# Optimization experiments

Hardware: AMD Instinct MI355X
Metric: run time of the kernel (lower is better)

Reference implementation:

```python
import jax, jax.numpy as jnp
import numpy as np

K = 1024      # num_embeddings
D = 256       # embedding_dim
BETA = 0.25


def setup_inputs() -> dict:
    key = jax.random.key(0)
    k1, k2 = jax.random.split(key)
    latents = jax.random.normal(k1, (32, D, 32, 32), dtype=jnp.float32)
    # nn.Embedding weight init: uniform(-1/K, 1/K)
    weight = jax.random.uniform(k2, (K, D), dtype=jnp.float32,
                                minval=-1.0 / K, maxval=1.0 / K)
    return {"latents": latents, "weight": weight}


def reference(latents, weight):
    # NCHW -> NHWC
    lat = jnp.transpose(latents, (0, 2, 3, 1))          # [B,H,W,D]
    lat_shape = lat.shape
    flat = lat.reshape(-1, D)                           # [N,D]

    dist = (jnp.sum(flat ** 2, axis=1, keepdims=True)
            - 2.0 * jnp.matmul(flat, weight.T)
            + jnp.sum(weight ** 2, axis=1))             # [N,K]

    min_ind = jnp.argmin(dist, axis=1)                  # [N]
    min_embed = jax.nn.one_hot(min_ind, K, dtype=flat.dtype)  # [N,K]

    # one-hot @ weight == direct gather
    z_q = jnp.take(weight, min_ind, axis=0).reshape(lat_shape)  # [B,H,W,D]

    sg = jax.lax.stop_gradient
    loss = (jnp.mean((sg(z_q) - lat) ** 2)
            + BETA * jnp.mean((z_q - sg(lat)) ** 2))

    # straight-through estimator
    z_q_st = lat + sg(z_q - lat)

    e_mean = jnp.mean(min_embed, axis=0)                # [K]
    perplexity = jnp.exp(-jnp.sum(e_mean * jnp.log(e_mean + 1e-10)))

    z_q_out = jnp.transpose(z_q_st, (0, 3, 1, 2))       # NHWC -> NCHW
    return (loss, z_q_out, perplexity, min_embed, min_ind[:, None])
```

## Files before the change

### kernel.cpp

```cpp
#include <hip/hip_runtime.h>

#define KN 1024
#define DD 256
#define NTOT 32768
#define HW 1024

#define OFF_LOSS 0
#define OFF_ZQ   1
#define OFF_PERP 8388609
#define OFF_EMB  8388610
#define OFF_IND  41943042

#define WS_WSUM2_OFF 4112
#define WS_WBH_OFF   8208
#define WS_WBL_OFF   (8208 + 524288)

#define XS_STRIDE 260
#define THR 3.0e-4f

typedef __bf16 bf16x8 __attribute__((ext_vector_type(8)));
typedef float  f32x4  __attribute__((ext_vector_type(4)));
typedef float  f32x2  __attribute__((ext_vector_type(2)));
typedef unsigned short ushort_t;

#define SM_XS    0
#define SM_XFH   33280
#define SM_XFL   49664
#define SM_WSC   66048
#define SM_PART  70144
#define SM_REDV  70144
#define SM_ROWM  71232
#define SM_CCNT  71360
#define SM_CLIST 71488
#define SM_FV    72512
#define SM_ASUM  73536
#define SM_BI    73664
#define SM_LRED  73792
#define SM_SIZE  73824

__device__ __forceinline__ unsigned short bf16_rne(float f) {
    unsigned u = __float_as_uint(f);
    return (unsigned short)((u + 0x7FFFu + ((u >> 16) & 1u)) >> 16);
}

__device__ __forceinline__ float exact_dist(const float* xs, const float* wsC,
                                            const float* asum,
                                            const float* __restrict__ w,
                                            int r, int k) {
    float a = 0.f;
    const float4* wr = (const float4*)(w + k * DD);
    const float4* xr = (const float4*)(xs + r * XS_STRIDE);
    #pragma unroll 4
    for (int q = 0; q < 64; ++q) {
        const float4 wv = wr[q];
        const float4 xv = xr[q];
        a = fmaf(xv.x, wv.x, a);
        a = fmaf(xv.y, wv.y, a);
        a = fmaf(xv.z, wv.z, a);
        a = fmaf(xv.w, wv.w, a);
    }
    return (asum[r] - 2.0f * a) + wsC[k];
}

__global__ __launch_bounds__(256) void vq_prep(const float* __restrict__ w,
                                               float* __restrict__ wsum2,
                                               ushort_t* __restrict__ wBh,
                                               ushort_t* __restrict__ wBl) {
    const int k = blockIdx.x;
    const int d = threadIdx.x;
    float v = w[k * DD + d];
    {
        const int c = k >> 4, s0 = d >> 5, g = (d >> 3) & 3, j = d & 7;
        const int lane = (k & 15) | (g << 4);
        const int idx = (((c * 8 + s0) * 64 + lane) << 3) + j;
        const unsigned short hh = bf16_rne(v);
        wBh[idx] = hh;
        wBl[idx] = bf16_rne(v - __uint_as_float((unsigned)hh << 16));
    }
    float s = v * v;
    #pragma unroll
    for (int off = 32; off; off >>= 1) s += __shfl_down(s, off, 64);
    __shared__ float wsum[4];
    const int wave = d >> 6, lane = d & 63;
    if (lane == 0) wsum[wave] = s;
    __syncthreads();
    if (d == 0) wsum2[k] = (wsum[0] + wsum[1]) + (wsum[2] + wsum[3]);
}

__global__ __launch_bounds__(512, 4) void vq_main(const float* __restrict__ lat,
                                                  const float* __restrict__ w,
                                                  const float* __restrict__ wsum2,
                                                  const ushort_t* __restrict__ wBh,
                                                  const ushort_t* __restrict__ wBl,
                                                  float* __restrict__ out,
                                                  unsigned* __restrict__ cnt,
                                                  double* __restrict__ lossSum) {
    extern __shared__ char smem[];
    float*    xs    = (float*)(smem + SM_XS);
    ushort_t* xfH   = (ushort_t*)(smem + SM_XFH);
    ushort_t* xfL   = (ushort_t*)(smem + SM_XFL);
    float*    wsC   = (float*)(smem + SM_WSC);
    float*    part  = (float*)(smem + SM_PART);
    float*    redv  = (float*)(smem + SM_REDV);
    float*    rowm  = (float*)(smem + SM_ROWM);
    unsigned* ccnt  = (unsigned*)(smem + SM_CCNT);
    int*      clist = (int*)(smem + SM_CLIST);
    float*    fv    = (float*)(smem + SM_FV);
    float*    asum  = (float*)(smem + SM_ASUM);
    int*      bi    = (int*)(smem + SM_BI);
    double*   lred  = (double*)(smem + SM_LRED);

    const int n0  = blockIdx.x * 32;
    const int b   = n0 >> 10;
    const int hw0 = n0 & 1023;
    const int tid = threadIdx.x;
    const int l   = tid & 63;
    const int wv  = tid >> 6;

    {
        const float* base = lat + (size_t)b * (DD * HW) + hw0;
        #pragma unroll
        for (int it = 0; it < 4; ++it) {
            const int u = it * 512 + tid;
            const int d = u >> 3, r4 = (u & 7) * 4;
            const f32x4 v = __builtin_nontemporal_load(
                reinterpret_cast<const f32x4*>(base + d * HW + r4));
            xs[(r4 + 0) * XS_STRIDE + d] = v.x;
            xs[(r4 + 1) * XS_STRIDE + d] = v.y;
            xs[(r4 + 2) * XS_STRIDE + d] = v.z;
            xs[(r4 + 3) * XS_STRIDE + d] = v.w;
        }
        wsC[tid] = wsum2[tid];
        wsC[tid + 512] = wsum2[tid + 512];
    }
    __syncthreads();

    #pragma unroll
    for (int h = 0; h < 2; ++h) {
        if (tid < 256) {
            const int r = tid & 15, seg = tid >> 4;
            float p = 0.f;
            #pragma unroll
            for (int i = 0; i < 16; ++i) {
                float x = xs[(h * 16 + r) * XS_STRIDE + seg * 16 + i];
                p += x * x;
            }
            part[seg * 17 + r] = p;
        }
        __syncthreads();
        if (tid < 16) {
            float a = 0.f;
            #pragma unroll
            for (int s = 0; s < 16; ++s) a += part[s * 17 + tid];
            asum[h * 16 + tid] = a;
        }
        __syncthreads();
    }

    #pragma unroll
    for (int i = 0; i < 2; ++i) {
        const int u  = tid + i * 512;
        const int rt = u >> 9, s0 = (u >> 6) & 7, ll = u & 63;
        const int row = rt * 16 + (ll & 15);
        const int d0  = s0 * 32 + (ll >> 4) * 8;
        const float4 x0 = *(const float4*)(xs + row * XS_STRIDE + d0);
        const float4 x1 = *(const float4*)(xs + row * XS_STRIDE + d0 + 4);
        float xv[8] = {x0.x, x0.y, x0.z, x0.w, x1.x, x1.y, x1.z, x1.w};
        unsigned hh[8], lo[8];
        #pragma unroll
        for (int j = 0; j < 8; ++j) {
            hh[j] = bf16_rne(xv[j]);
            lo[j] = bf16_rne(xv[j] - __uint_as_float(hh[j] << 16));
        }
        uint4 ph, pl;
        ph.x = hh[0] | (hh[1] << 16); ph.y = hh[2] | (hh[3] << 16);
        ph.z = hh[4] | (hh[5] << 16); ph.w = hh[6] | (hh[7] << 16);
        pl.x = lo[0] | (lo[1] << 16); pl.y = lo[2] | (lo[3] << 16);
        pl.z = lo[4] | (lo[5] << 16); pl.w = lo[6] | (lo[7] << 16);
        *(uint4*)(xfH + u * 8) = ph;
        *(uint4*)(xfL + u * 8) = pl;
    }
    __syncthreads();

    f32x4 acc[2][8];
    #pragma unroll
    for (int rt = 0; rt < 2; ++rt)
        #pragma unroll
        for (int c = 0; c < 8; ++c)
            acc[rt][c] = (f32x4){0.f, 0.f, 0.f, 0.f};

    {
        bf16x8 ah0, ah1, al0, al1;
        bf16x8 pbh0, pbl0, pbh1, pbl1;

        #define BOFF(s0_, c_) (((size_t)(((wv * 8 + (c_)) * 8 + (s0_)) * 64 + l)) * 8)
        pbh0 = *(const bf16x8*)(wBh + BOFF(0, 0));
        pbl0 = *(const bf16x8*)(wBl + BOFF(0, 0));
        pbh1 = *(const bf16x8*)(wBh + BOFF(0, 1));
        pbl1 = *(const bf16x8*)(wBl + BOFF(0, 1));

        #pragma unroll
        for (int it = 0; it < 64; ++it) {
            const int s0 = it >> 3, c = it & 7;
            if (c == 0) {
                ah0 = *(const bf16x8*)(xfH + ((0 * 8 + s0) * 64 + l) * 8);
                ah1 = *(const bf16x8*)(xfH + ((1 * 8 + s0) * 64 + l) * 8);
                al0 = *(const bf16x8*)(xfL + ((0 * 8 + s0) * 64 + l) * 8);
                al1 = *(const bf16x8*)(xfL + ((1 * 8 + s0) * 64 + l) * 8);
            }
            bf16x8 bh, bl;
            if ((it & 1) == 0) { bh = pbh0; bl = pbl0; } else { bh = pbh1; bl = pbl1; }
            if (it + 2 < 64) {
                const int nit = it + 2, ns = nit >> 3, nc = nit & 7;
                if ((it & 1) == 0) {
                    pbh0 = *(const bf16x8*)(wBh + BOFF(ns, nc));
                    pbl0 = *(const bf16x8*)(wBl + BOFF(ns, nc));
                } else {
                    pbh1 = *(const bf16x8*)(wBh + BOFF(ns, nc));
                    pbl1 = *(const bf16x8*)(wBl + BOFF(ns, nc));
                }
            }
            acc[0][c] = __builtin_amdgcn_mfma_f32_16x16x32_bf16(ah0, bh, acc[0][c], 0, 0, 0);
            acc[1][c] = __builtin_amdgcn_mfma_f32_16x16x32_bf16(ah1, bh, acc[1][c], 0, 0, 0);
            acc[0][c] = __builtin_amdgcn_mfma_f32_16x16x32_bf16(ah0, bl, acc[0][c], 0, 0, 0);
            acc[1][c] = __builtin_amdgcn_mfma_f32_16x16x32_bf16(ah1, bl, acc[1][c], 0, 0, 0);
            acc[0][c] = __builtin_amdgcn_mfma_f32_16x16x32_bf16(al0, bh, acc[0][c], 0, 0, 0);
            acc[1][c] = __builtin_amdgcn_mfma_f32_16x16x32_bf16(al1, bh, acc[1][c], 0, 0, 0);
        }
        #undef BOFF
    }

    float rmv[2][4];
    #pragma unroll
    for (int rt = 0; rt < 2; ++rt)
        #pragma unroll
        for (int q = 0; q < 4; ++q) rmv[rt][q] = 3.4e38f;
    #pragma unroll
    for (int c = 0; c < 8; ++c) {
        const float cv = wsC[(wv * 8 + c) * 16 + (l & 15)];
        #pragma unroll
        for (int rt = 0; rt < 2; ++rt) {
            #pragma unroll
            for (int q = 0; q < 4; ++q) {
                const float dv = fmaf(-2.0f, acc[rt][c][q], cv);
                acc[rt][c][q] = dv;
                rmv[rt][q] = fminf(rmv[rt][q], dv);
            }
        }
    }
    #pragma unroll
    for (int rt = 0; rt < 2; ++rt)
        #pragma unroll
        for (int q = 0; q < 4; ++q) {
            float m = rmv[rt][q];
            #pragma unroll
            for (int off = 1; off < 16; off <<= 1) m = fminf(m, __shfl_xor(m, off, 64));
            rmv[rt][q] = m;
        }
    if ((l & 15) == 0) {
        const int g = l >> 4;
        #pragma unroll
        for (int rt = 0; rt < 2; ++rt)
            #pragma unroll
            for (int q = 0; q < 4; ++q)
                redv[wv * 32 + rt * 16 + g * 4 + q] = rmv[rt][q];
    }
    __syncthreads();
    if (tid < 32) {
        float m = redv[tid];
        #pragma unroll
        for (int ww = 1; ww < 8; ++ww) m = fminf(m, redv[ww * 32 + tid]);
        rowm[tid] = m;
        ccnt[tid] = 0u;
    }
    __syncthreads();

    #pragma unroll
    for (int rt = 0; rt < 2; ++rt) {
        #pragma unroll
        for (int q = 0; q < 4; ++q) {
            const int row = rt * 16 + ((l >> 4) << 2) + q;
            const float lim = rowm[row] + THR;
            #pragma unroll
            for (int c = 0; c < 8; ++c) {
                if (acc[rt][c][q] <= lim) {
                    const unsigned pos = atomicAdd(&ccnt[row], 1u);
                    if (pos < 8) clist[row * 8 + pos] = (wv * 8 + c) * 16 + (l & 15);
                }
            }
        }
    }
    __syncthreads();

    if (tid < 256) {
        const int r = tid >> 3, ci = tid & 7;
        const unsigned cc = ccnt[r];
        if (cc >= 2u) {
            if (cc <= 8u) {
                if ((unsigned)ci < cc)
                    fv[r * 8 + ci] = exact_dist(xs, wsC, asum, w, r, clist[r * 8 + ci]);
            } else {
                float bvv = 3.4e38f; int bkk = ci * 128;
                for (int k = ci * 128; k < ci * 128 + 128; ++k) {
                    const float dvv = exact_dist(xs, wsC, asum, w, r, k);
                    if (dvv < bvv) { bvv = dvv; bkk = k; }
                }
                fv[r * 8 + ci] = bvv;
                clist[r * 8 + ci] = bkk;
            }
        }
    }
    __syncthreads();
    if (tid < 32) {
        const unsigned cc = ccnt[tid];
        int kk;
        if (cc == 1u) kk = clist[tid * 8];
        else {
            const unsigned ncand = (cc <= 8u) ? cc : 8u;
            float v = fv[tid * 8]; kk = clist[tid * 8];
            for (unsigned ci = 1; ci < ncand; ++ci) {
                const float ov = fv[tid * 8 + ci];
                const int   ok = clist[tid * 8 + ci];
                if (ov < v || (ov == v && ok < kk)) { v = ov; kk = ok; }
            }
        }
        bi[tid] = kk;
        __builtin_nontemporal_store((float)kk, &out[OFF_IND + n0 + tid]);
        atomicAdd(&cnt[kk], 1u);
    }
    __syncthreads();

    {
        float* zq_out = out + OFF_ZQ + (size_t)b * (DD * HW) + hw0;
        #pragma unroll
        for (int it = 0; it < 8; ++it) {
            const int u = it * 512 + tid;
            const int d = u >> 4, j2 = (u & 15) * 2;
            const float la0 = xs[(j2 + 0) * XS_STRIDE + d];
            const float la1 = xs[(j2 + 1) * XS_STRIDE + d];
            const float z0  = w[bi[j2 + 0] * DD + d];
            const float z1  = w[bi[j2 + 1] * DD + d];
            f32x2 v;
            v.x = la0 + (z0 - la0);
            v.y = la1 + (z1 - la1);
            __builtin_nontemporal_store(v, reinterpret_cast<f32x2*>(zq_out + d * HW + j2));
        }
    }

    {
        f32x2* emb2 = reinterpret_cast<f32x2*>(out + OFF_EMB) + (size_t)n0 * (KN / 2);
        #pragma unroll
        for (int it = 0; it < 32; ++it) {
            const int f = it * 512 + tid;
            const int r = f >> 9;
            const int kq = (f & 511) * 2;
            const int tt = bi[r];
            f32x2 v2;
            v2.x = (kq     == tt) ? 1.0f : 0.0f;
            v2.y = (kq + 1 == tt) ? 1.0f : 0.0f;
            __builtin_nontemporal_store(v2, &emb2[f]);
        }
    }

    #pragma unroll
    for (int h = 0; h < 2; ++h) {
        if (tid < 256) {
            const int jj = tid & 15, db = tid >> 4;
            const int krow = bi[h * 16 + jj];
            float lsum = 0.f;
            #pragma unroll
            for (int it = 0; it < 16; ++it) {
                const int d = it * 16 + db;
                const float latv = xs[(h * 16 + jj) * XS_STRIDE + d];
                const float zq   = w[krow * DD + d];
                const float dif  = zq - latv;
                lsum = fmaf(dif, dif, lsum);
            }
            float s2 = lsum;
            #pragma unroll
            for (int off = 32; off; off >>= 1) s2 += __shfl_down(s2, off, 64);
            if ((tid & 63) == 0) lred[wv] = (double)s2;
        }
        __syncthreads();
        if (tid == 0) {
            double t = (lred[0] + lred[1]) + (lred[2] + lred[3]);
            atomicAdd(lossSum, t);
        }
        __syncthreads();
    }
}

__global__ __launch_bounds__(1024) void vq_finalize(const unsigned* __restrict__ cnt,
                                                    const double* __restrict__ lossSum,
                                                    float* __restrict__ out) {
    const int t = threadIdx.x;
    __shared__ float red[16];
    const float e = (float)cnt[t] * (1.0f / 32768.0f);
    float s = e * logf(e + 1e-10f);
    #pragma unroll
    for (int off = 32; off; off >>= 1) s += __shfl_down(s, off, 64);
    const int wave = t >> 6, lane = t & 63;
    if (lane == 0) red[wave] = s;
    __syncthreads();
    if (t == 0) {
        float tot = 0.f;
        #pragma unroll
        for (int i = 0; i < 16; ++i) tot += red[i];
        out[OFF_PERP] = expf(-tot);
        const float m = (float)(lossSum[0] * (1.0 / 8388608.0));
        out[OFF_LOSS] = m + 0.25f * m;
    }
}

extern "C" void kernel_launch(void* const* d_in, const int* in_sizes, int n_in,
                              void* d_out, int out_size, void* d_ws, size_t ws_size,
                              hipStream_t stream) {
    const float* lat = (const float*)d_in[0];
    const float* w   = (const float*)d_in[1];

    char* ws = (char*)d_ws;
    double*   lossSum = (double*)ws;
    unsigned* cnt     = (unsigned*)(ws + 8);
    float*    wsum2   = (float*)(ws + WS_WSUM2_OFF);
    ushort_t* wBh     = (ushort_t*)(ws + WS_WBH_OFF);
    ushort_t* wBl     = (ushort_t*)(ws + WS_WBL_OFF);
    float*    out     = (float*)d_out;

    (void)hipMemsetAsync(d_ws, 0, 4104, stream);

    (void)hipFuncSetAttribute(reinterpret_cast<const void*>(vq_main),
                              hipFuncAttributeMaxDynamicSharedMemorySize, SM_SIZE);

    vq_prep<<<KN, 256, 0, stream>>>(w, wsum2, wBh, wBl);
    vq_main<<<NTOT / 32, 512, SM_SIZE, stream>>>(lat, w, wsum2, wBh, wBl, out, cnt, lossSum);
    vq_finalize<<<1, 1024, 0, stream>>>(cnt, lossSum, out);
}
```

Baseline: 129.6 us.

## Drop low bf16 half of codebook and widen candidate margin by row L1 norm

The codebook is now split into a single bf16 term instead of a high/low pair, so each distance step issues 4 MFMAs instead of 6 and reads half the codebook bytes. To make up for the larger error of the approximate distance, the candidate threshold now grows with each row's L1 norm (computed alongside the squared norm). Candidates are then re-checked with exact fp32 distances, as before. The B prefetch becomes a 3-deep rotation. The risk is more rows with many candidates, which means more exact rechecks or fallback work. That could eat into the gain or affect correctness if the bound is too tight.

```diff
diff --git a/kernel.cpp b/kernel.cpp
--- a/kernel.cpp
+++ b/kernel.cpp
@@ -13,10 +13,8 @@
 
 #define WS_WSUM2_OFF 4112
 #define WS_WBH_OFF   8208
-#define WS_WBL_OFF   (8208 + 524288)
 
 #define XS_STRIDE 260
-#define THR 3.0e-4f
 
 typedef __bf16 bf16x8 __attribute__((ext_vector_type(8)));
 typedef float  f32x4  __attribute__((ext_vector_type(4)));
@@ -36,7 +34,9 @@
 #define SM_ASUM  73536
 #define SM_BI    73664
 #define SM_LRED  73792
-#define SM_SIZE  73824
+#define SM_PART2 73824
+#define SM_SABS  74912
+#define SM_SIZE  75040
 
 __device__ __forceinline__ unsigned short bf16_rne(float f) {
     unsigned u = __float_as_uint(f);
@@ -64,8 +64,7 @@
 
 __global__ __launch_bounds__(256) void vq_prep(const float* __restrict__ w,
                                                float* __restrict__ wsum2,
-                                               ushort_t* __restrict__ wBh,
-                                               ushort_t* __restrict__ wBl) {
+                                               ushort_t* __restrict__ wBh) {
     const int k = blockIdx.x;
     const int d = threadIdx.x;
     float v = w[k * DD + d];
@@ -73,9 +72,7 @@
         const int c = k >> 4, s0 = d >> 5, g = (d >> 3) & 3, j = d & 7;
         const int lane = (k & 15) | (g << 4);
         const int idx = (((c * 8 + s0) * 64 + lane) << 3) + j;
-        const unsigned short hh = bf16_rne(v);
-        wBh[idx] = hh;
-        wBl[idx] = bf16_rne(v - __uint_as_float((unsigned)hh << 16));
+        wBh[idx] = bf16_rne(v);
     }
     float s = v * v;
     #pragma unroll
@@ -91,7 +88,6 @@
                                                   const float* __restrict__ w,
                                                   const float* __restrict__ wsum2,
                                                   const ushort_t* __restrict__ wBh,
-                                                  const ushort_t* __restrict__ wBl,
                                                   float* __restrict__ out,
                                                   unsigned* __restrict__ cnt,
                                                   double* __restrict__ lossSum) {
@@ -101,12 +97,14 @@
     ushort_t* xfL   = (ushort_t*)(smem + SM_XFL);
     float*    wsC   = (float*)(smem + SM_WSC);
     float*    part  = (float*)(smem + SM_PART);
+    float*    part2 = (float*)(smem + SM_PART2);
     float*    redv  = (float*)(smem + SM_REDV);
     float*    rowm  = (float*)(smem + SM_ROWM);
     unsigned* ccnt  = (unsigned*)(smem + SM_CCNT);
     int*      clist = (int*)(smem + SM_CLIST);
     float*    fv    = (float*)(smem + SM_FV);
     float*    asum  = (float*)(smem + SM_ASUM);
+    float*    sabs  = (float*)(smem + SM_SABS);
     int*      bi    = (int*)(smem + SM_BI);
     double*   lred  = (double*)(smem + SM_LRED);
 
@@ -139,20 +137,23 @@
     for (int h = 0; h < 2; ++h) {
         if (tid < 256) {
             const int r = tid & 15, seg = tid >> 4;
-            float p = 0.f;
+            float p = 0.f, pa = 0.f;
             #pragma unroll
             for (int i = 0; i < 16; ++i) {
                 float x = xs[(h * 16 + r) * XS_STRIDE + seg * 16 + i];
                 p += x * x;
+                pa += fabsf(x);
             }
             part[seg * 17 + r] = p;
+            part2[seg * 17 + r] = pa;
         }
         __syncthreads();
         if (tid < 16) {
-            float a = 0.f;
-            #pragma unroll
-            for (int s = 0; s < 16; ++s) a += part[s * 17 + tid];
+            float a = 0.f, sa = 0.f;
+            #pragma unroll
+            for (int s = 0; s < 16; ++s) { a += part[s * 17 + tid]; sa += part2[s * 17 + tid]; }
             asum[h * 16 + tid] = a;
+            sabs[h * 16 + tid] = sa;
         }
         __syncthreads();
     }
@@ -191,13 +192,12 @@
 
     {
         bf16x8 ah0, ah1, al0, al1;
-        bf16x8 pbh0, pbl0, pbh1, pbl1;
+        bf16x8 pb0, pb1, pb2;
 
         #define BOFF(s0_, c_) (((size_t)(((wv * 8 + (c_)) * 8 + (s0_)) * 64 + l)) * 8)
-        pbh0 = *(const bf16x8*)(wBh + BOFF(0, 0));
-        pbl0 = *(const bf16x8*)(wBl + BOFF(0, 0));
-        pbh1 = *(const bf16x8*)(wBh + BOFF(0, 1));
-        pbl1 = *(const bf16x8*)(wBl + BOFF(0, 1));
+        pb0 = *(const bf16x8*)(wBh + BOFF(0, 0));
+        pb1 = *(const bf16x8*)(wBh + BOFF(0, 1));
+        pb2 = *(const bf16x8*)(wBh + BOFF(0, 2));
 
         #pragma unroll
         for (int it = 0; it < 64; ++it) {
@@ -208,22 +208,23 @@
                 al0 = *(const bf16x8*)(xfL + ((0 * 8 + s0) * 64 + l) * 8);
                 al1 = *(const bf16x8*)(xfL + ((1 * 8 + s0) * 64 + l) * 8);
             }
-            bf16x8 bh, bl;
-            if ((it & 1) == 0) { bh = pbh0; bl = pbl0; } else { bh = pbh1; bl = pbl1; }
-            if (it + 2 < 64) {
-                const int nit = it + 2, ns = nit >> 3, nc = nit & 7;
-                if ((it & 1) == 0) {
-                    pbh0 = *(const bf16x8*)(wBh + BOFF(ns, nc));
-                    pbl0 = *(const bf16x8*)(wBl + BOFF(ns, nc));
-                } else {
-                    pbh1 = *(const bf16x8*)(wBh + BOFF(ns, nc));
-                    pbl1 = *(const bf16x8*)(wBl + BOFF(ns, nc));
+            bf16x8 bh;
+            switch (it % 3) {
+                case 0:  bh = pb0; break;
+                case 1:  bh = pb1; break;
+                default: bh = pb2; break;
+            }
+            const int nit = it + 3;
+            if (nit < 64) {
+                const int ns = nit >> 3, nc = nit & 7;
+                switch (it % 3) {
+                    case 0:  pb0 = *(const bf16x8*)(wBh + BOFF(ns, nc)); break;
+                    case 1:  pb1 = *(const bf16x8*)(wBh + BOFF(ns, nc)); break;
+                    default: pb2 = *(const bf16x8*)(wBh + BOFF(ns, nc)); break;
                 }
             }
             acc[0][c] = __builtin_amdgcn_mfma_f32_16x16x32_bf16(ah0, bh, acc[0][c], 0, 0, 0);
             acc[1][c] = __builtin_amdgcn_mfma_f32_16x16x32_bf16(ah1, bh, acc[1][c], 0, 0, 0);
-            acc[0][c] = __builtin_amdgcn_mfma_f32_16x16x32_bf16(ah0, bl, acc[0][c], 0, 0, 0);
-            acc[1][c] = __builtin_amdgcn_mfma_f32_16x16x32_bf16(ah1, bl, acc[1][c], 0, 0, 0);
             acc[0][c] = __builtin_amdgcn_mfma_f32_16x16x32_bf16(al0, bh, acc[0][c], 0, 0, 0);
             acc[1][c] = __builtin_amdgcn_mfma_f32_16x16x32_bf16(al1, bh, acc[1][c], 0, 0, 0);
         }
@@ -270,7 +271,7 @@
         float m = redv[tid];
         #pragma unroll
         for (int ww = 1; ww < 8; ++ww) m = fminf(m, redv[ww * 32 + tid]);
-        rowm[tid] = m;
+        rowm[tid] = m + fmaf(7.6e-6f, sabs[tid], 3.0e-4f);
         ccnt[tid] = 0u;
     }
     __syncthreads();
@@ -280,7 +281,7 @@
         #pragma unroll
         for (int q = 0; q < 4; ++q) {
             const int row = rt * 16 + ((l >> 4) << 2) + q;
-            const float lim = rowm[row] + THR;
+            const float lim = rowm[row];
             #pragma unroll
             for (int c = 0; c < 8; ++c) {
                 if (acc[rt][c][q] <= lim) {
@@ -423,7 +424,6 @@
     unsigned* cnt     = (unsigned*)(ws + 8);
     float*    wsum2   = (float*)(ws + WS_WSUM2_OFF);
     ushort_t* wBh     = (ushort_t*)(ws + WS_WBH_OFF);
-    ushort_t* wBl     = (ushort_t*)(ws + WS_WBL_OFF);
     float*    out     = (float*)d_out;
 
     (void)hipMemsetAsync(d_ws, 0, 4104, stream);
@@ -431,7 +431,7 @@
     (void)hipFuncSetAttribute(reinterpret_cast<const void*>(vq_main),
                               hipFuncAttributeMaxDynamicSharedMemorySize, SM_SIZE);
 
-    vq_prep<<<KN, 256, 0, stream>>>(w, wsum2, wBh, wBl);
-    vq_main<<<NTOT / 32, 512, SM_SIZE, stream>>>(lat, w, wsum2, wBh, wBl, out, cnt, lossSum);
+    vq_prep<<<KN, 256, 0, stream>>>(w, wsum2, wBh);
+    vq_main<<<NTOT / 32, 512, SM_SIZE, stream>>>(lat, w, wsum2, wBh, out, cnt, lossSum);
     vq_finalize<<<1, 1024, 0, stream>>>(cnt, lossSum, out);
 }
```

New measurement: 385.6 us. +197.6%, slower.
